# Optimization experiments

Hardware: AMD Instinct MI355X
Metric: run time of the kernel (lower is better)

## Reference

```python
import jax, jax.numpy as jnp
import numpy as np

N, E, B = 30000, 300000, 64
F_N, F_E, F_G, H = 64, 32, 32, 64
EPS = 1e-5


def _bn(t, gamma, beta):
    # BatchNorm1d in training mode: biased batch statistics over the row dim.
    m = t.mean(axis=0)
    v = t.var(axis=0)
    return gamma * (t - m) * jax.lax.rsqrt(v + EPS) + beta


def _seg_mean(vals, idx, num):
    s = jax.ops.segment_sum(vals, idx, num_segments=num)
    c = jax.ops.segment_sum(jnp.ones((vals.shape[0], 1), vals.dtype), idx,
                            num_segments=num)
    return s / jnp.maximum(c, 1.0)


def setup_inputs() -> dict:
    key = jax.random.key(0)
    ks = jax.random.split(key, 32)
    inp = {
        'x': jax.random.normal(ks[0], (N, F_N), jnp.float32),
        'edge_index': jax.random.randint(ks[1], (2, E), 0, N),
        'e': jax.random.normal(ks[2], (E, F_E), jnp.float32),
        'u': jax.random.normal(ks[3], (B, F_G), jnp.float32),
        'batch': jnp.sort(jax.random.randint(ks[4], (N,), 0, B)),
        'g_node': jnp.ones((F_N,), jnp.float32),
        'b_node': jnp.zeros((F_N,), jnp.float32),
        'g_edge': jnp.ones((F_E,), jnp.float32),
        'b_edge': jnp.zeros((F_E,), jnp.float32),
        'g_glob': jnp.ones((F_G,), jnp.float32),
        'b_glob': jnp.zeros((F_G,), jnp.float32),
    }
    # Per-step Linear weights; input dims follow the feature-size threading in __init__.
    din_e = [2 * F_N + F_E + F_G, 3 * H + H, 3 * H + H]  # [192, 256, 256]
    din_n = [F_N + H + F_G, H + H + H, H + H + H]        # [160, 192, 192]
    din_g = [H + F_G, H + H, H + H]                      # [96, 128, 128]
    k = 5
    for l in range(3):
        for tag, din in (('e', din_e[l]), ('n', din_n[l]), ('g', din_g[l])):
            inp[f'W{tag}{l}'] = jax.random.normal(ks[k], (din, H), jnp.float32) / np.sqrt(din)
            inp[f'b{tag}{l}'] = jnp.zeros((H,), jnp.float32)
            k += 1
    return inp


def _forward(x, e, u, batch, src, dst,
             g_node, b_node, g_edge, b_edge, g_glob, b_glob,
             We, be, Wn, bn, Wg, bg):
    # Input normalization
    x = _bn(x, g_node, b_node)
    e = _bn(e, g_edge, b_edge)
    u = _bn(u, g_glob, b_glob)
    for l in range(3):
        # Edge model: per-edge MLP over [x_src, x_dst, e, u_edge]
        e_in = jnp.concatenate([x[src], x[dst], e, u[batch[src]]], axis=-1)
        e = jax.nn.relu(e_in @ We[l] + be[l])
        # Node model: aggregate incoming messages at destination (mean)
        agg = _seg_mean(e, dst, N)
        n_in = jnp.concatenate([x, agg, u[batch]], axis=-1)
        x = jax.nn.relu(n_in @ Wn[l] + bn[l])
        # Global model: mean-pool nodes per graph
        g_in = jnp.concatenate([_seg_mean(x, batch, B), u], axis=-1)
        u = jax.nn.relu(g_in @ Wg[l] + bg[l])
    return x, e, u


def reference(x, edge_index, e, u, batch,
              g_node, b_node, g_edge, b_edge, g_glob, b_glob,
              We0, be0, Wn0, bn0, Wg0, bg0,
              We1, be1, Wn1, bn1, Wg1, bg1,
              We2, be2, Wn2, bn2, Wg2, bg2):
    src, dst = edge_index[0], edge_index[1]
    We = (We0, We1, We2); be = (be0, be1, be2)
    Wn = (Wn0, Wn1, Wn2); bn = (bn0, bn1, bn2)
    Wg = (Wg0, Wg1, Wg2); bg = (bg0, bg1, bg2)
    return _forward(x, e, u, batch, src, dst,
                    g_node, b_node, g_edge, b_edge, g_glob, b_glob,
                    We, be, Wn, bn, Wg, bg)
```

## Files before the change

### kernel.cpp

```cpp
#include <hip/hip_runtime.h>
#include <hip/hip_bf16.h>

#define EPS 1e-5f
typedef __hip_bfloat16 bf16;
typedef __attribute__((ext_vector_type(8))) short  short8;
typedef __attribute__((ext_vector_type(4))) float  f32x4;

__device__ __forceinline__ float b2f(bf16 v) { return __bfloat162float(v); }
__device__ __forceinline__ float bs2f(short s) { bf16 b = *reinterpret_cast<bf16*>(&s); return b2f(b); }
__device__ __forceinline__ float ldv(const void* p, size_t i, bool bf) {
    return bf ? b2f(((const bf16*)p)[i]) : ((const float*)p)[i];
}
__device__ __forceinline__ void stv(void* p, size_t i, float v, bool bf) {
    if (bf) ((bf16*)p)[i] = __float2bfloat16(v);
    else    ((float*)p)[i] = v;
}
__device__ __forceinline__ short f2bs(float v) {
    bf16 b = __float2bfloat16(v);
    return *reinterpret_cast<short*>(&b);
}
__device__ __forceinline__ short8 ld16s(const short* p) { return *(const short8*)p; }

__global__ void detect_dtype(const unsigned short* __restrict__ xs, float* __restrict__ flag) {
    __shared__ int cnt;
    if (threadIdx.x == 0) cnt = 0;
    __syncthreads();
    unsigned short u = xs[threadIdx.x];
    int e = (u >> 7) & 0xFF;
    int sane = (u == 0 || (e >= 110 && e <= 140)) ? 1 : 0;
    atomicAdd(&cnt, sane);
    __syncthreads();
    if (threadIdx.x == 0) flag[0] = (cnt >= 230) ? 1.0f : 0.0f;
}

template<int C>
__global__ __launch_bounds__(256) void bn_stats(const void* __restrict__ in, int R,
                                                float* __restrict__ stats, const float* __restrict__ flag) {
    bool isbf = flag[0] != 0.f;
    const int RG = 256 / C;
    int c = threadIdx.x % C, rg = threadIdx.x / C;
    float s = 0.f, s2 = 0.f;
    if (isbf) {
        const bf16* ip = (const bf16*)in;
        for (int r = blockIdx.x * RG + rg; r < R; r += gridDim.x * RG) {
            float v = b2f(ip[(size_t)r * C + c]); s += v; s2 += v * v;
        }
    } else {
        const float* ip = (const float*)in;
        for (int r = blockIdx.x * RG + rg; r < R; r += gridDim.x * RG) {
            float v = ip[(size_t)r * C + c]; s += v; s2 += v * v;
        }
    }
    __shared__ float sm[2][256];
    sm[0][threadIdx.x] = s; sm[1][threadIdx.x] = s2;
    __syncthreads();
    if (threadIdx.x < C) {
        float ts = 0.f, t2 = 0.f;
        for (int g = 0; g < RG; g++) { ts += sm[0][g * C + c]; t2 += sm[1][g * C + c]; }
        atomicAdd(&stats[c], ts);
        atomicAdd(&stats[C + c], t2);
    }
}

__global__ __launch_bounds__(256) void bn_apply_x(const void* __restrict__ in, short* __restrict__ out,
                                                  const float* __restrict__ stats, int R,
                                                  const void* __restrict__ gamma, const void* __restrict__ beta,
                                                  const float* __restrict__ flag) {
    bool isbf = flag[0] != 0.f;
    int total = R * 64;
    for (int i = blockIdx.x * 256 + threadIdx.x; i < total; i += gridDim.x * 256) {
        int c = i & 63;
        float mean = stats[c] / (float)R;
        float var = stats[64 + c] / (float)R - mean * mean;
        float inv = rsqrtf(var + EPS);
        out[i] = f2bs(ldv(gamma, c, isbf) * (ldv(in, i, isbf) - mean) * inv + ldv(beta, c, isbf));
    }
}

__global__ __launch_bounds__(256) void bn_apply_u(const void* __restrict__ in, float* __restrict__ outf,
                                                  short* __restrict__ outb,
                                                  const float* __restrict__ stats, int R,
                                                  const void* __restrict__ gamma, const void* __restrict__ beta,
                                                  const float* __restrict__ flag) {
    bool isbf = flag[0] != 0.f;
    int total = R * 32;
    for (int i = blockIdx.x * 256 + threadIdx.x; i < total; i += gridDim.x * 256) {
        int c = i & 31;
        float mean = stats[c] / (float)R;
        float var = stats[32 + c] / (float)R - mean * mean;
        float inv = rsqrtf(var + EPS);
        float v = ldv(gamma, c, isbf) * (ldv(in, i, isbf) - mean) * inv + ldv(beta, c, isbf);
        outf[i] = v; outb[i] = f2bs(v);
    }
}

__global__ __launch_bounds__(256) void count_kernel(const int* __restrict__ ei, int* __restrict__ cnt, int E) {
    int stride = gridDim.x * 256;
    for (int t = blockIdx.x * 256 + threadIdx.x; t < E; t += stride) atomicAdd(&cnt[ei[E + t]], 1);
}

__global__ __launch_bounds__(256) void csr_offsets(const int* __restrict__ cnt, int* __restrict__ off,
                                                   int* __restrict__ wcur, int* __restrict__ cursor, int N,
                                                   const int* __restrict__ batch, int* __restrict__ gstart, int B) {
    int n = blockIdx.x * 256 + threadIdx.x;
    if (n < N) {
        int o = atomicAdd(cursor, cnt[n]);
        off[n] = o; wcur[n] = o;
    }
    if (blockIdx.x == 0 && threadIdx.x <= B) {
        int t = threadIdx.x;
        int lo = 0, hi = N;
        while (lo < hi) { int mid = (lo + hi) >> 1; if (batch[mid] < t) lo = mid + 1; else hi = mid; }
        gstart[t] = lo;
    }
}

__global__ __launch_bounds__(256) void csr_fill(const int* __restrict__ ei, int* __restrict__ wcur,
                                                int* __restrict__ csr, int E) {
    int stride = gridDim.x * 256;
    for (int t = blockIdx.x * 256 + threadIdx.x; t < E; t += stride) {
        int d = ei[E + t];
        int pos = atomicAdd(&wcur[d], 1);
        csr[pos] = t;
    }
}

__global__ __launch_bounds__(256) void transpose_w(
    const void* __restrict__ W0, const void* __restrict__ W1, const void* __restrict__ W2,
    const void* __restrict__ W3, const void* __restrict__ W4, const void* __restrict__ W5,
    short* __restrict__ out, const float* __restrict__ flag)
{
    bool isbf = flag[0] != 0.f;
    const void* Ws[6] = {W0, W1, W2, W3, W4, W5};
    const int   din[6] = {192, 256, 256, 160, 192, 192};
    int mtx = blockIdx.x >> 3;
    int off = 0;
    for (int i = 0; i < mtx; i++) off += 64 * din[i];
    int d = din[mtx];
    const void* W = Ws[mtx];
    for (int i = (blockIdx.x & 7) * 256 + threadIdx.x; i < 64 * d; i += 8 * 256) {
        int n = i / d, k = i % d;
        out[off + n * d + k] = f2bs(ldv(W, (size_t)k * 64 + n, isbf));
    }
}

template<bool L0>
__global__ __launch_bounds__(256) void edge_mfma(
    const int* __restrict__ ei, const int* __restrict__ batchv,
    const short* __restrict__ xb,
    const void* __restrict__ ein, size_t ein_off,
    const float* __restrict__ estats, const void* __restrict__ egamma, const void* __restrict__ ebeta,
    const short* __restrict__ ub,
    const short* __restrict__ Wt, const void* __restrict__ biasv,
    void* __restrict__ eout, size_t eout_off,
    int E, const float* __restrict__ flag,
    int ein_force_bf, int eout_force_bf, short* __restrict__ eout2)
{
    constexpr int DIN = L0 ? 192 : 256;
    constexpr int NQ = DIN / 32;
    constexpr int ROWB = DIN * 2;
    __shared__ __align__(16) char Wl[64 * ROWB];
    __shared__ __align__(16) char T[4 * 2048];
    const bool isbf = flag[0] != 0.f;
    const bool ein_bf = ein_force_bf ? true : isbf;
    const bool eout_bf = eout_force_bf ? true : isbf;
    const int w = threadIdx.x >> 6, j = threadIdx.x & 63;
    const int m16 = j & 15, c8v = j >> 4, c8 = c8v * 8;
    const int rr8 = j >> 3, cc8 = j & 7;

    for (int i = threadIdx.x; i < DIN * 8; i += 256) {
        int lin = i * 16;
        int row = i / (DIN / 8);
        *(short8*)(Wl + (lin ^ ((row & 7) << 4))) = *(const short8*)(Wt + i * 8);
    }
    __syncthreads();

    char* Tw = T + w * 2048;
    const int wkey = (m16 & 7) << 4;

    float sc[8], sh[8];
    if constexpr (L0) {
        #pragma unroll
        for (int k = 0; k < 8; k++) {
            int col = c8 + k;
            float m = estats[col] / (float)E;
            float iv = rsqrtf(estats[32 + col] / (float)E - m * m + EPS);
            sc[k] = ldv(egamma, col, isbf) * iv;
            sh[k] = ldv(ebeta, col, isbf) - m * sc[k];
        }
    }
    float bc[4];
    #pragma unroll
    for (int t = 0; t < 4; t++) bc[t] = ldv(biasv, t * 16 + m16, isbf);

    const int ntiles = (E + 63) >> 6;
    const int gs = gridDim.x;
    int tile = blockIdx.x;
    if (tile < ntiles) {
        int ec = tile * 64 + w * 16 + m16; if (ec > E - 1) ec = E - 1;
        int s = ei[ec], d = ei[E + ec];
        for (; tile < ntiles; tile += gs) {
            const int ecC = ec, sC = s, dC = d;
            const int tn = tile + gs;
            if (tn < ntiles) {
                int e2 = tn * 64 + w * 16 + m16; if (e2 > E - 1) e2 = E - 1;
                ec = e2; s = ei[e2]; d = ei[E + e2];
            }
            int g = batchv[sC];

            short8 af[NQ];
            af[0] = ld16s(xb + (size_t)sC * 64 + c8);
            af[1] = ld16s(xb + (size_t)sC * 64 + 32 + c8);
            af[2] = ld16s(xb + (size_t)dC * 64 + c8);
            af[3] = ld16s(xb + (size_t)dC * 64 + 32 + c8);
            if constexpr (L0) {
                float ev[8];
                if (isbf) {
                    short8 r = ld16s((const short*)ein + (size_t)ecC * 32 + c8);
                    #pragma unroll
                    for (int k = 0; k < 8; k++) ev[k] = bs2f(r[k]);
                } else {
                    const float* ef = (const float*)ein + (size_t)ecC * 32 + c8;
                    float4 a = *(const float4*)ef, b = *(const float4*)(ef + 4);
                    ev[0]=a.x; ev[1]=a.y; ev[2]=a.z; ev[3]=a.w; ev[4]=b.x; ev[5]=b.y; ev[6]=b.z; ev[7]=b.w;
                }
                #pragma unroll
                for (int k = 0; k < 8; k++) af[4][k] = f2bs(ev[k] * sc[k] + sh[k]);
                af[5] = ld16s(ub + (size_t)g * 32 + c8);
            } else {
                if (ein_bf) {
                    af[4] = ld16s((const short*)ein + ein_off + (size_t)ecC * 64 + c8);
                    af[5] = ld16s((const short*)ein + ein_off + (size_t)ecC * 64 + 32 + c8);
                } else {
                    const float* ef = (const float*)ein + ein_off + (size_t)ecC * 64;
                    float4 a = *(const float4*)(ef + c8), b = *(const float4*)(ef + c8 + 4);
                    af[4][0]=f2bs(a.x); af[4][1]=f2bs(a.y); af[4][2]=f2bs(a.z); af[4][3]=f2bs(a.w);
                    af[4][4]=f2bs(b.x); af[4][5]=f2bs(b.y); af[4][6]=f2bs(b.z); af[4][7]=f2bs(b.w);
                    a = *(const float4*)(ef + 32 + c8); b = *(const float4*)(ef + 36 + c8);
                    af[5][0]=f2bs(a.x); af[5][1]=f2bs(a.y); af[5][2]=f2bs(a.z); af[5][3]=f2bs(a.w);
                    af[5][4]=f2bs(b.x); af[5][5]=f2bs(b.y); af[5][6]=f2bs(b.z); af[5][7]=f2bs(b.w);
                }
                af[6] = ld16s(ub + (size_t)g * 64 + c8);
                af[7] = ld16s(ub + (size_t)g * 64 + 32 + c8);
            }

            f32x4 acc[4] = {{0,0,0,0},{0,0,0,0},{0,0,0,0},{0,0,0,0}};
            #pragma unroll
            for (int q = 0; q < NQ; q++) {
                #pragma unroll
                for (int t = 0; t < 4; t++) {
                    int lin = (t * 16 + m16) * ROWB + q * 64 + c8v * 16;
                    short8 bv = *(const short8*)(Wl + (lin ^ wkey));
                    acc[t] = __builtin_amdgcn_mfma_f32_16x16x32_bf16(af[q], bv, acc[t], 0, 0, 0);
                }
            }

            const int we = tile * 64 + w * 16;
            #pragma unroll
            for (int t = 0; t < 4; t++) {
                #pragma unroll
                for (int r = 0; r < 4; r++) {
                    float v = fmaxf(acc[t][r] + bc[t], 0.f);
                    int rr = c8v * 4 + r;
                    int lin = rr * 128 + (t * 16 + m16) * 2;
                    *(short*)(Tw + (lin ^ ((rr & 7) << 4))) = f2bs(v);
                }
            }
            #pragma unroll
            for (int i = 0; i < 2; i++) {
                int r = i * 8 + rr8;
                int e2 = we + r;
                if (e2 < E) {
                    short8 row = *(const short8*)(Tw + ((r * 128 + cc8 * 16) ^ ((rr8 & 7) << 4)));
                    if (eout_bf) {
                        *(short8*)((short*)eout + eout_off + (size_t)e2 * 64 + cc8 * 8) = row;
                    } else {
                        float* op = (float*)eout + eout_off + (size_t)e2 * 64 + cc8 * 8;
                        float4 a, b;
                        a.x=bs2f(row[0]); a.y=bs2f(row[1]); a.z=bs2f(row[2]); a.w=bs2f(row[3]);
                        b.x=bs2f(row[4]); b.y=bs2f(row[5]); b.z=bs2f(row[6]); b.w=bs2f(row[7]);
                        *(float4*)op = a; *(float4*)(op + 4) = b;
                    }
                    if (eout2) {
                        *(short8*)(eout2 + (size_t)e2 * 64 + cc8 * 8) = row;
                    }
                }
            }
        }
    }
}

template<bool L0, bool FINAL>
__global__ __launch_bounds__(256) void node_fused(
    const int* __restrict__ batchv, const short* __restrict__ xin,
    const int* __restrict__ off, const int* __restrict__ csr, const int* __restrict__ cntv,
    const void* __restrict__ eout, size_t eoff,
    const short* __restrict__ ub,
    const short* __restrict__ Wt, const void* __restrict__ biasv,
    short* __restrict__ xoutb, void* __restrict__ dout, int N,
    const float* __restrict__ flag, int e_force_bf)
{
    constexpr int DIN = L0 ? 160 : 192;
    constexpr int NQ = DIN / 32;
    constexpr int ROWB = DIN * 2;
    __shared__ __align__(16) char Wl[64 * ROWB];
    __shared__ __align__(16) char T[4 * 2048];
    const bool isbf = flag[0] != 0.f;
    const bool e_bf = e_force_bf ? true : isbf;
    const int w = threadIdx.x >> 6, j = threadIdx.x & 63;
    const int m16 = j & 15, c8v = j >> 4, c8 = c8v * 8;
    const int rr8 = j >> 3, cc8 = j & 7;
    const int nb = blockIdx.x * 64 + w * 16;

    for (int i = threadIdx.x; i < DIN * 8; i += 256) {
        int lin = i * 16;
        int row = i / (DIN / 8);
        *(short8*)(Wl + (lin ^ ((row & 7) << 4))) = *(const short8*)(Wt + i * 8);
    }
    __syncthreads();

    char* Tw = T + w * 2048;
    const int wkey = (m16 & 7) << 4;

    int n = nb + m16; if (n > N - 1) n = N - 1;
    int g = batchv[n];

    short8 af[NQ];
    af[0] = ld16s(xin + (size_t)n * 64 + c8);
    af[1] = ld16s(xin + (size_t)n * 64 + 32 + c8);

    {
        int st = off[n], c = cntv[n];
        float s0[8] = {0,0,0,0,0,0,0,0}, s1[8] = {0,0,0,0,0,0,0,0};
        int t = 0;
        if (e_bf) {
            const short* ep = (const short*)eout + eoff;
            for (; t + 2 <= c; t += 2) {
                int e0 = csr[st + t], e1 = csr[st + t + 1];
                short8 r0 = ld16s(ep + (size_t)e0 * 64 + c8);
                short8 q0 = ld16s(ep + (size_t)e0 * 64 + 32 + c8);
                short8 r1 = ld16s(ep + (size_t)e1 * 64 + c8);
                short8 q1 = ld16s(ep + (size_t)e1 * 64 + 32 + c8);
                #pragma unroll
                for (int k = 0; k < 8; k++) { s0[k] += bs2f(r0[k]) + bs2f(r1[k]); s1[k] += bs2f(q0[k]) + bs2f(q1[k]); }
            }
            if (t < c) {
                int e0 = csr[st + t];
                short8 r0 = ld16s(ep + (size_t)e0 * 64 + c8);
                short8 q0 = ld16s(ep + (size_t)e0 * 64 + 32 + c8);
                #pragma unroll
                for (int k = 0; k < 8; k++) { s0[k] += bs2f(r0[k]); s1[k] += bs2f(q0[k]); }
            }
        } else {
            const float* ep = (const float*)eout + eoff;
            for (; t < c; t++) {
                int e0 = csr[st + t];
                const float* rp = ep + (size_t)e0 * 64;
                float4 a = *(const float4*)(rp + c8), b = *(const float4*)(rp + c8 + 4);
                float4 x = *(const float4*)(rp + 32 + c8), y = *(const float4*)(rp + 36 + c8);
                s0[0]+=a.x; s0[1]+=a.y; s0[2]+=a.z; s0[3]+=a.w; s0[4]+=b.x; s0[5]+=b.y; s0[6]+=b.z; s0[7]+=b.w;
                s1[0]+=x.x; s1[1]+=x.y; s1[2]+=x.z; s1[3]+=x.w; s1[4]+=y.x; s1[5]+=y.y; s1[6]+=y.z; s1[7]+=y.w;
            }
        }
        float rc = 1.0f / fmaxf((float)c, 1.0f);
        #pragma unroll
        for (int k = 0; k < 8; k++) { af[2][k] = f2bs(s0[k] * rc); af[3][k] = f2bs(s1[k] * rc); }
    }

    if constexpr (L0) {
        af[4] = ld16s(ub + (size_t)g * 32 + c8);
    } else {
        af[4] = ld16s(ub + (size_t)g * 64 + c8);
        af[5] = ld16s(ub + (size_t)g * 64 + 32 + c8);
    }

    f32x4 acc[4] = {{0,0,0,0},{0,0,0,0},{0,0,0,0},{0,0,0,0}};
    #pragma unroll
    for (int q = 0; q < NQ; q++) {
        #pragma unroll
        for (int t = 0; t < 4; t++) {
            int lin = (t * 16 + m16) * ROWB + q * 64 + c8v * 16;
            short8 bv = *(const short8*)(Wl + (lin ^ wkey));
            acc[t] = __builtin_amdgcn_mfma_f32_16x16x32_bf16(af[q], bv, acc[t], 0, 0, 0);
        }
    }

    #pragma unroll
    for (int t = 0; t < 4; t++) {
        float bcv = ldv(biasv, t * 16 + m16, isbf);
        #pragma unroll
        for (int r = 0; r < 4; r++) {
            float v = fmaxf(acc[t][r] + bcv, 0.f);
            int rr = c8v * 4 + r;
            int lin = rr * 128 + (t * 16 + m16) * 2;
            *(short*)(Tw + (lin ^ ((rr & 7) << 4))) = f2bs(v);
        }
    }
    #pragma unroll
    for (int i = 0; i < 2; i++) {
        int r = i * 8 + rr8;
        int n2 = nb + r;
        if (n2 < N) {
            short8 row = *(const short8*)(Tw + ((r * 128 + cc8 * 16) ^ ((rr8 & 7) << 4)));
            *(short8*)&xoutb[(size_t)n2 * 64 + cc8 * 8] = row;
            if (FINAL) {
                if (isbf) {
                    *(short8*)((short*)dout + (size_t)n2 * 64 + cc8 * 8) = row;
                } else {
                    float* op = (float*)dout + (size_t)n2 * 64 + cc8 * 8;
                    float4 a, b;
                    a.x=bs2f(row[0]); a.y=bs2f(row[1]); a.z=bs2f(row[2]); a.w=bs2f(row[3]);
                    b.x=bs2f(row[4]); b.y=bs2f(row[5]); b.z=bs2f(row[6]); b.w=bs2f(row[7]);
                    *(float4*)op = a; *(float4*)(op + 4) = b;
                }
            }
        }
    }
}

__global__ __launch_bounds__(256) void pool_kernel(const int* __restrict__ gstart,
                                                   const short* __restrict__ xb,
                                                   float* __restrict__ gsum) {
    int g = blockIdx.x >> 3, slice = blockIdx.x & 7;
    int st = gstart[g], en = gstart[g + 1];
    int len = en - st;
    int K = (len + 7) >> 3;
    int b0 = st + slice * K;
    int b1 = min(b0 + K, en);
    int rg = threadIdx.x >> 3, cc8 = threadIdx.x & 7;
    float a[8] = {0,0,0,0,0,0,0,0};
    for (int r = b0 + rg; r < b1; r += 32) {
        short8 v = *(const short8*)&xb[(size_t)r * 64 + cc8 * 8];
        #pragma unroll
        for (int k = 0; k < 8; k++) a[k] += bs2f(v[k]);
    }
    __shared__ float sm[32][64];
    #pragma unroll
    for (int k = 0; k < 8; k++) sm[rg][cc8 * 8 + k] = a[k];
    __syncthreads();
    if (threadIdx.x < 64) {
        float s = 0.f;
        #pragma unroll 8
        for (int q = 0; q < 32; q++) s += sm[q][threadIdx.x];
        atomicAdd(&gsum[g * 64 + threadIdx.x], s);
    }
}

template<int FU>
__global__ __launch_bounds__(256) void glob_gemm(
    const int* __restrict__ gstart, const float* __restrict__ gsum,
    const float* __restrict__ uin,
    const void* __restrict__ W, const void* __restrict__ biasv,
    float* __restrict__ uoutf, short* __restrict__ uoutb,
    const float* __restrict__ flag)
{
    bool isbf = flag[0] != 0.f;
    const int DIN = 64 + FU;
    __shared__ float s[4][192];
    int w = threadIdx.x >> 6, j = threadIdx.x & 63;
    int g = blockIdx.x * 4 + w;
    int st = gstart[g], en = gstart[g + 1];
    float rc = 1.0f / fmaxf((float)(en - st), 1.0f);
    s[w][j] = gsum[g * 64 + j] * rc;
    if (j < FU) s[w][64 + j] = uin[g * FU + j];
    float acc = ldv(biasv, j, isbf);
    for (int k = 0; k < DIN; k++) acc += s[w][k] * ldv(W, (size_t)k * 64 + j, isbf);
    acc = fmaxf(acc, 0.f);
    uoutf[g * 64 + j] = acc;
    uoutb[g * 64 + j] = f2bs(acc);
}

__global__ __launch_bounds__(256) void cast_out(const float* __restrict__ in, void* __restrict__ out,
                                                size_t out_off, int n, const float* __restrict__ flag) {
    bool isbf = flag[0] != 0.f;
    for (int i = blockIdx.x * 256 + threadIdx.x; i < n; i += gridDim.x * 256)
        stv(out, out_off + i, in[i], isbf);
}

extern "C" void kernel_launch(void* const* d_in, const int* in_sizes, int n_in,
                              void* d_out, int out_size, void* d_ws, size_t ws_size,
                              hipStream_t stream) {
    const void* x_in   = d_in[0];
    const int*  ei     = (const int*)d_in[1];
    const void* e_raw  = d_in[2];
    const void* u_raw  = d_in[3];
    const int*  batchv = (const int*)d_in[4];
    const void *g_node = d_in[5],  *b_node = d_in[6];
    const void *g_edge = d_in[7],  *b_edge = d_in[8];
    const void *g_glob = d_in[9],  *b_glob = d_in[10];
    const void* We[3] = {d_in[11], d_in[17], d_in[23]};
    const void* be[3] = {d_in[12], d_in[18], d_in[24]};
    const void* Wn[3] = {d_in[13], d_in[19], d_in[25]};
    const void* bn[3] = {d_in[14], d_in[20], d_in[26]};
    const void* Wg[3] = {d_in[15], d_in[21], d_in[27]};
    const void* bg[3] = {d_in[16], d_in[22], d_in[28]};

    const int N = in_sizes[0] / 64;
    const int E = in_sizes[2] / 32;
    const int B = in_sizes[3] / 32;

    float* p = (float*)d_ws;
    float* zbase  = p;
    float* stats  = p; p += 3 * 128;
    int*   cursor = (int*)p; p += 4;
    int*   cnt    = (int*)p; p += N;
    float* gsum0  = p; p += B * 64;
    float* gsum1  = p; p += B * 64;
    float* gsum2  = p; p += B * 64;
    size_t zbytes = (size_t)((char*)p - (char*)zbase);
    float* dflag  = p; p += 4;
    float* uN     = p; p += B * 32;
    float* uA     = p; p += B * 64;
    float* uB     = p; p += B * 64;
    int*   off    = (int*)p; p += N;
    int*   wcur   = (int*)p; p += N;
    int*   gstart = (int*)p; p += 72;
    int*   csr    = (int*)p; p += E;
    short* xb0    = (short*)p; p += (size_t)N * 32;
    short* xb1    = (short*)p; p += (size_t)N * 32;
    short* ubN    = (short*)p; p += B * 16;
    short* ubA    = (short*)p; p += B * 32;
    short* ubB    = (short*)p; p += B * 32;
    short* WtAll  = (short*)p; p += 79872 / 2;
    const short* WtE0 = WtAll;
    const short* WtE1 = WtAll + 12288;
    const short* WtE2 = WtAll + 28672;
    const short* WtN0 = WtAll + 45056;
    const short* WtN1 = WtAll + 55296;
    const short* WtN2 = WtAll + 67584;

    short* eb16 = nullptr;
    {
        size_t used = (size_t)((char*)p - (char*)d_ws);
        used = (used + 15) & ~(size_t)15;
        size_t need = used + (size_t)E * 64 * sizeof(short);
        if (ws_size >= need) eb16 = (short*)((char*)d_ws + used);
    }

    const size_t EOFF = (size_t)N * 64;
    const size_t UOFF = EOFF + (size_t)E * 64;

    hipMemsetAsync(zbase, 0, zbytes, stream);

    detect_dtype<<<1, 256, 0, stream>>>((const unsigned short*)x_in, dflag);

    bn_stats<64><<<256, 256, 0, stream>>>(x_in, N, stats, dflag);
    bn_stats<32><<<512, 256, 0, stream>>>(e_raw, E, stats + 128, dflag);
    bn_stats<32><<<8,   256, 0, stream>>>(u_raw, B, stats + 256, dflag);
    bn_apply_x<<<512, 256, 0, stream>>>(x_in, xb0, stats, N, g_node, b_node, dflag);
    bn_apply_u<<<8,   256, 0, stream>>>(u_raw, uN, ubN, stats + 256, B, g_glob, b_glob, dflag);
    count_kernel<<<512, 256, 0, stream>>>(ei, cnt, E);
    csr_offsets<<<(N + 255) / 256, 256, 0, stream>>>(cnt, off, wcur, cursor, N, batchv, gstart, B);
    csr_fill<<<512, 256, 0, stream>>>(ei, wcur, csr, E);
    transpose_w<<<48, 256, 0, stream>>>(We[0], We[1], We[2], Wn[0], Wn[1], Wn[2], WtAll, dflag);

    const int NG = (N + 63) / 64;
    const int NT = (E + 63) / 64;
    const int EG0 = NT < 1280 ? NT : 1280;
    const int EG  = NT < 1024 ? NT : 1024;

    if (eb16) {
        edge_mfma<true><<<EG0, 256, 0, stream>>>(
            ei, batchv, xb0, e_raw, 0, stats + 128, g_edge, b_edge,
            ubN, WtE0, be[0], eb16, 0, E, dflag, 0, 1, nullptr);
        node_fused<true, false><<<NG, 256, 0, stream>>>(
            batchv, xb0, off, csr, cnt, eb16, 0, ubN, WtN0, bn[0], xb1, nullptr, N, dflag, 1);
        pool_kernel<<<B * 8, 256, 0, stream>>>(gstart, xb1, gsum0);
        glob_gemm<32><<<B / 4, 256, 0, stream>>>(gstart, gsum0, uN, Wg[0], bg[0], uA, ubA, dflag);

        edge_mfma<false><<<EG, 256, 0, stream>>>(
            ei, batchv, xb1, eb16, 0, nullptr, nullptr, nullptr,
            ubA, WtE1, be[1], eb16, 0, E, dflag, 1, 1, nullptr);
        node_fused<false, false><<<NG, 256, 0, stream>>>(
            batchv, xb1, off, csr, cnt, eb16, 0, ubA, WtN1, bn[1], xb0, nullptr, N, dflag, 1);
        pool_kernel<<<B * 8, 256, 0, stream>>>(gstart, xb0, gsum1);
        glob_gemm<64><<<B / 4, 256, 0, stream>>>(gstart, gsum1, uA, Wg[1], bg[1], uB, ubB, dflag);

        edge_mfma<false><<<EG, 256, 0, stream>>>(
            ei, batchv, xb0, eb16, 0, nullptr, nullptr, nullptr,
            ubB, WtE2, be[2], d_out, EOFF, E, dflag, 1, 0, eb16);
        node_fused<false, true><<<NG, 256, 0, stream>>>(
            batchv, xb0, off, csr, cnt, eb16, 0, ubB, WtN2, bn[2], xb1, d_out, N, dflag, 1);
        pool_kernel<<<B * 8, 256, 0, stream>>>(gstart, xb1, gsum2);
        glob_gemm<64><<<B / 4, 256, 0, stream>>>(gstart, gsum2, uB, Wg[2], bg[2], uA, ubA, dflag);
    } else {
        edge_mfma<true><<<EG0, 256, 0, stream>>>(
            ei, batchv, xb0, e_raw, 0, stats + 128, g_edge, b_edge,
            ubN, WtE0, be[0], d_out, EOFF, E, dflag, 0, 0, nullptr);
        node_fused<true, false><<<NG, 256, 0, stream>>>(
            batchv, xb0, off, csr, cnt, d_out, EOFF, ubN, WtN0, bn[0], xb1, nullptr, N, dflag, 0);
        pool_kernel<<<B * 8, 256, 0, stream>>>(gstart, xb1, gsum0);
        glob_gemm<32><<<B / 4, 256, 0, stream>>>(gstart, gsum0, uN, Wg[0], bg[0], uA, ubA, dflag);

        edge_mfma<false><<<EG, 256, 0, stream>>>(
            ei, batchv, xb1, d_out, EOFF, nullptr, nullptr, nullptr,
            ubA, WtE1, be[1], d_out, EOFF, E, dflag, 0, 0, nullptr);
        node_fused<false, false><<<NG, 256, 0, stream>>>(
            batchv, xb1, off, csr, cnt, d_out, EOFF, ubA, WtN1, bn[1], xb0, nullptr, N, dflag, 0);
        pool_kernel<<<B * 8, 256, 0, stream>>>(gstart, xb0, gsum1);
        glob_gemm<64><<<B / 4, 256, 0, stream>>>(gstart, gsum1, uA, Wg[1], bg[1], uB, ubB, dflag);

        edge_mfma<false><<<EG, 256, 0, stream>>>(
            ei, batchv, xb0, d_out, EOFF, nullptr, nullptr, nullptr,
            ubB, WtE2, be[2], d_out, EOFF, E, dflag, 0, 0, nullptr);
        node_fused<false, true><<<NG, 256, 0, stream>>>(
            batchv, xb0, off, csr, cnt, d_out, EOFF, ubB, WtN2, bn[2], xb1, d_out, N, dflag, 0);
        pool_kernel<<<B * 8, 256, 0, stream>>>(gstart, xb1, gsum2);
        glob_gemm<64><<<B / 4, 256, 0, stream>>>(gstart, gsum2, uB, Wg[2], bg[2], uA, ubA, dflag);
    }

    cast_out<<<16, 256, 0, stream>>>(uA, d_out, UOFF, B * 64, dflag);
}
```

Baseline: 481.2 us.

## Process edges in destination-sorted CSR order so node aggregation reads contiguously

Builds permuted source/destination index arrays in CSR (destination-sorted) order and runs the edge kernels over that order on the bf16 path. Edge features are kept in sorted order in the scratch buffer, and the final layer scatters rows back to the original edge order for output. Node aggregation then reads each node's incoming edges as a contiguous block instead of through indirect CSR lookups. The cost is one extra permutation kernel, a gather of the raw edge features in the first layer, and a scattered write in the last layer.

```diff
diff --git a/kernel.cpp b/kernel.cpp
--- a/kernel.cpp
+++ b/kernel.cpp
@@ -122,6 +122,16 @@
         int d = ei[E + t];
         int pos = atomicAdd(&wcur[d], 1);
         csr[pos] = t;
+    }
+}
+
+__global__ __launch_bounds__(256) void perm_build(const int* __restrict__ ei, const int* __restrict__ csr,
+                                                  int* __restrict__ sp, int* __restrict__ dp, int E) {
+    int stride = gridDim.x * 256;
+    for (int t = blockIdx.x * 256 + threadIdx.x; t < E; t += stride) {
+        int e0 = csr[t];
+        sp[t] = ei[e0];
+        dp[t] = ei[E + e0];
     }
 }
 
@@ -146,7 +156,9 @@
 
 template<bool L0>
 __global__ __launch_bounds__(256) void edge_mfma(
-    const int* __restrict__ ei, const int* __restrict__ batchv,
+    const int* __restrict__ sp, const int* __restrict__ dp,
+    const int* __restrict__ csrv,
+    const int* __restrict__ batchv,
     const short* __restrict__ xb,
     const void* __restrict__ ein, size_t ein_off,
     const float* __restrict__ estats, const void* __restrict__ egamma, const void* __restrict__ ebeta,
@@ -154,7 +166,7 @@
     const short* __restrict__ Wt, const void* __restrict__ biasv,
     void* __restrict__ eout, size_t eout_off,
     int E, const float* __restrict__ flag,
-    int ein_force_bf, int eout_force_bf, short* __restrict__ eout2)
+    int ein_force_bf, int eout_force_bf, int eout_orig, short* __restrict__ eout2)
 {
     constexpr int DIN = L0 ? 192 : 256;
     constexpr int NQ = DIN / 32;
@@ -198,13 +210,16 @@
     int tile = blockIdx.x;
     if (tile < ntiles) {
         int ec = tile * 64 + w * 16 + m16; if (ec > E - 1) ec = E - 1;
-        int s = ei[ec], d = ei[E + ec];
+        int s = sp[ec], d = dp[ec];
+        int eo = ec;
+        if constexpr (L0) { if (csrv) eo = csrv[ec]; }
         for (; tile < ntiles; tile += gs) {
-            const int ecC = ec, sC = s, dC = d;
+            const int ecC = ec, sC = s, dC = d, eoC = eo;
             const int tn = tile + gs;
             if (tn < ntiles) {
                 int e2 = tn * 64 + w * 16 + m16; if (e2 > E - 1) e2 = E - 1;
-                ec = e2; s = ei[e2]; d = ei[E + e2];
+                ec = e2; s = sp[e2]; d = dp[e2];
+                if constexpr (L0) { if (csrv) eo = csrv[e2]; }
             }
             int g = batchv[sC];
 
@@ -216,11 +231,11 @@
             if constexpr (L0) {
                 float ev[8];
                 if (isbf) {
-                    short8 r = ld16s((const short*)ein + (size_t)ecC * 32 + c8);
+                    short8 r = ld16s((const short*)ein + (size_t)eoC * 32 + c8);
                     #pragma unroll
                     for (int k = 0; k < 8; k++) ev[k] = bs2f(r[k]);
                 } else {
-                    const float* ef = (const float*)ein + (size_t)ecC * 32 + c8;
+                    const float* ef = (const float*)ein + (size_t)eoC * 32 + c8;
                     float4 a = *(const float4*)ef, b = *(const float4*)(ef + 4);
                     ev[0]=a.x; ev[1]=a.y; ev[2]=a.z; ev[3]=a.w; ev[4]=b.x; ev[5]=b.y; ev[6]=b.z; ev[7]=b.w;
                 }
@@ -272,10 +287,11 @@
                 int e2 = we + r;
                 if (e2 < E) {
                     short8 row = *(const short8*)(Tw + ((r * 128 + cc8 * 16) ^ ((rr8 & 7) << 4)));
+                    int rowIdx = (eout_orig && csrv) ? csrv[e2] : e2;
                     if (eout_bf) {
-                        *(short8*)((short*)eout + eout_off + (size_t)e2 * 64 + cc8 * 8) = row;
+                        *(short8*)((short*)eout + eout_off + (size_t)rowIdx * 64 + cc8 * 8) = row;
                     } else {
-                        float* op = (float*)eout + eout_off + (size_t)e2 * 64 + cc8 * 8;
+                        float* op = (float*)eout + eout_off + (size_t)rowIdx * 64 + cc8 * 8;
                         float4 a, b;
                         a.x=bs2f(row[0]); a.y=bs2f(row[1]); a.z=bs2f(row[2]); a.w=bs2f(row[3]);
                         b.x=bs2f(row[4]); b.y=bs2f(row[5]); b.z=bs2f(row[6]); b.w=bs2f(row[7]);
@@ -298,7 +314,7 @@
     const short* __restrict__ ub,
     const short* __restrict__ Wt, const void* __restrict__ biasv,
     short* __restrict__ xoutb, void* __restrict__ dout, int N,
-    const float* __restrict__ flag, int e_force_bf)
+    const float* __restrict__ flag, int e_force_bf, int contig)
 {
     constexpr int DIN = L0 ? 160 : 192;
     constexpr int NQ = DIN / 32;
@@ -332,28 +348,47 @@
     {
         int st = off[n], c = cntv[n];
         float s0[8] = {0,0,0,0,0,0,0,0}, s1[8] = {0,0,0,0,0,0,0,0};
-        int t = 0;
         if (e_bf) {
             const short* ep = (const short*)eout + eoff;
-            for (; t + 2 <= c; t += 2) {
-                int e0 = csr[st + t], e1 = csr[st + t + 1];
-                short8 r0 = ld16s(ep + (size_t)e0 * 64 + c8);
-                short8 q0 = ld16s(ep + (size_t)e0 * 64 + 32 + c8);
-                short8 r1 = ld16s(ep + (size_t)e1 * 64 + c8);
-                short8 q1 = ld16s(ep + (size_t)e1 * 64 + 32 + c8);
-                #pragma unroll
-                for (int k = 0; k < 8; k++) { s0[k] += bs2f(r0[k]) + bs2f(r1[k]); s1[k] += bs2f(q0[k]) + bs2f(q1[k]); }
-            }
-            if (t < c) {
-                int e0 = csr[st + t];
-                short8 r0 = ld16s(ep + (size_t)e0 * 64 + c8);
-                short8 q0 = ld16s(ep + (size_t)e0 * 64 + 32 + c8);
-                #pragma unroll
-                for (int k = 0; k < 8; k++) { s0[k] += bs2f(r0[k]); s1[k] += bs2f(q0[k]); }
+            if (contig) {
+                const short* base = ep + (size_t)st * 64;
+                int t = 0;
+                for (; t + 2 <= c; t += 2) {
+                    short8 r0 = ld16s(base + (size_t)t * 64 + c8);
+                    short8 q0 = ld16s(base + (size_t)t * 64 + 32 + c8);
+                    short8 r1 = ld16s(base + (size_t)(t + 1) * 64 + c8);
+                    short8 q1 = ld16s(base + (size_t)(t + 1) * 64 + 32 + c8);
+                    #pragma unroll
+                    for (int k = 0; k < 8; k++) { s0[k] += bs2f(r0[k]) + bs2f(r1[k]); s1[k] += bs2f(q0[k]) + bs2f(q1[k]); }
+                }
+                if (t < c) {
+                    short8 r0 = ld16s(base + (size_t)t * 64 + c8);
+                    short8 q0 = ld16s(base + (size_t)t * 64 + 32 + c8);
+                    #pragma unroll
+                    for (int k = 0; k < 8; k++) { s0[k] += bs2f(r0[k]); s1[k] += bs2f(q0[k]); }
+                }
+            } else {
+                int t = 0;
+                for (; t + 2 <= c; t += 2) {
+                    int e0 = csr[st + t], e1 = csr[st + t + 1];
+                    short8 r0 = ld16s(ep + (size_t)e0 * 64 + c8);
+                    short8 q0 = ld16s(ep + (size_t)e0 * 64 + 32 + c8);
+                    short8 r1 = ld16s(ep + (size_t)e1 * 64 + c8);
+                    short8 q1 = ld16s(ep + (size_t)e1 * 64 + 32 + c8);
+                    #pragma unroll
+                    for (int k = 0; k < 8; k++) { s0[k] += bs2f(r0[k]) + bs2f(r1[k]); s1[k] += bs2f(q0[k]) + bs2f(q1[k]); }
+                }
+                if (t < c) {
+                    int e0 = csr[st + t];
+                    short8 r0 = ld16s(ep + (size_t)e0 * 64 + c8);
+                    short8 q0 = ld16s(ep + (size_t)e0 * 64 + 32 + c8);
+                    #pragma unroll
+                    for (int k = 0; k < 8; k++) { s0[k] += bs2f(r0[k]); s1[k] += bs2f(q0[k]); }
+                }
             }
         } else {
             const float* ep = (const float*)eout + eoff;
-            for (; t < c; t++) {
+            for (int t = 0; t < c; t++) {
                 int e0 = csr[st + t];
                 const float* rp = ep + (size_t)e0 * 64;
                 float4 a = *(const float4*)(rp + c8), b = *(const float4*)(rp + c8 + 4);
@@ -516,6 +551,8 @@
     int*   wcur   = (int*)p; p += N;
     int*   gstart = (int*)p; p += 72;
     int*   csr    = (int*)p; p += E;
+    int*   sp     = (int*)p; p += E;
+    int*   dp     = (int*)p; p += E;
     short* xb0    = (short*)p; p += (size_t)N * 32;
     short* xb1    = (short*)p; p += (size_t)N * 32;
     short* ubN    = (short*)p; p += B * 16;
@@ -552,6 +589,7 @@
     count_kernel<<<512, 256, 0, stream>>>(ei, cnt, E);
     csr_offsets<<<(N + 255) / 256, 256, 0, stream>>>(cnt, off, wcur, cursor, N, batchv, gstart, B);
     csr_fill<<<512, 256, 0, stream>>>(ei, wcur, csr, E);
+    perm_build<<<512, 256, 0, stream>>>(ei, csr, sp, dp, E);
     transpose_w<<<48, 256, 0, stream>>>(We[0], We[1], We[2], Wn[0], Wn[1], Wn[2], WtAll, dflag);
 
     const int NG = (N + 63) / 64;
@@ -561,50 +599,50 @@
 
     if (eb16) {
         edge_mfma<true><<<EG0, 256, 0, stream>>>(
-            ei, batchv, xb0, e_raw, 0, stats + 128, g_edge, b_edge,
-            ubN, WtE0, be[0], eb16, 0, E, dflag, 0, 1, nullptr);
+            sp, dp, csr, batchv, xb0, e_raw, 0, stats + 128, g_edge, b_edge,
+            ubN, WtE0, be[0], eb16, 0, E, dflag, 0, 1, 0, nullptr);
         node_fused<true, false><<<NG, 256, 0, stream>>>(
-            batchv, xb0, off, csr, cnt, eb16, 0, ubN, WtN0, bn[0], xb1, nullptr, N, dflag, 1);
+            batchv, xb0, off, csr, cnt, eb16, 0, ubN, WtN0, bn[0], xb1, nullptr, N, dflag, 1, 1);
         pool_kernel<<<B * 8, 256, 0, stream>>>(gstart, xb1, gsum0);
         glob_gemm<32><<<B / 4, 256, 0, stream>>>(gstart, gsum0, uN, Wg[0], bg[0], uA, ubA, dflag);
 
         edge_mfma<false><<<EG, 256, 0, stream>>>(
-            ei, batchv, xb1, eb16, 0, nullptr, nullptr, nullptr,
-            ubA, WtE1, be[1], eb16, 0, E, dflag, 1, 1, nullptr);
+            sp, dp, csr, batchv, xb1, eb16, 0, nullptr, nullptr, nullptr,
+            ubA, WtE1, be[1], eb16, 0, E, dflag, 1, 1, 0, nullptr);
         node_fused<false, false><<<NG, 256, 0, stream>>>(
-            batchv, xb1, off, csr, cnt, eb16, 0, ubA, WtN1, bn[1], xb0, nullptr, N, dflag, 1);
+            batchv, xb1, off, csr, cnt, eb16, 0, ubA, WtN1, bn[1], xb0, nullptr, N, dflag, 1, 1);
         pool_kernel<<<B * 8, 256, 0, stream>>>(gstart, xb0, gsum1);
         glob_gemm<64><<<B / 4, 256, 0, stream>>>(gstart, gsum1, uA, Wg[1], bg[1], uB, ubB, dflag);
 
         edge_mfma<false><<<EG, 256, 0, stream>>>(
-            ei, batchv, xb0, eb16, 0, nullptr, nullptr, nullptr,
-            ubB, WtE2, be[2], d_out, EOFF, E, dflag, 1, 0, eb16);
+            sp, dp, csr, batchv, xb0, eb16, 0, nullptr, nullptr, nullptr,
+            ubB, WtE2, be[2], d_out, EOFF, E, dflag, 1, 0, 1, eb16);
         node_fused<false, true><<<NG, 256, 0, stream>>>(
-            batchv, xb0, off, csr, cnt, eb16, 0, ubB, WtN2, bn[2], xb1, d_out, N, dflag, 1);
+            batchv, xb0, off, csr, cnt, eb16, 0, ubB, WtN2, bn[2], xb1, d_out, N, dflag, 1, 1);
         pool_kernel<<<B * 8, 256, 0, stream>>>(gstart, xb1, gsum2);
         glob_gemm<64><<<B / 4, 256, 0, stream>>>(gstart, gsum2, uB, Wg[2], bg[2], uA, ubA, dflag);
     } else {
         edge_mfma<true><<<EG0, 256, 0, stream>>>(
-            ei, batchv, xb0, e_raw, 0, stats + 128, g_edge, b_edge,
-            ubN, WtE0, be[0], d_out, EOFF, E, dflag, 0, 0, nullptr);
+            ei, ei + E, nullptr, batchv, xb0, e_raw, 0, stats + 128, g_edge, b_edge,
+            ubN, WtE0, be[0], d_out, EOFF, E, dflag, 0, 0, 0, nullptr);
         node_fused<true, false><<<NG, 256, 0, stream>>>(
-            batchv, xb0, off, csr, cnt, d_out, EOFF, ubN, WtN0, bn[0], xb1, nullptr, N, dflag, 0);
+            batchv, xb0, off, csr, cnt, d_out, EOFF, ubN, WtN0, bn[0], xb1, nullptr, N, dflag, 0, 0);
         pool_kernel<<<B * 8, 256, 0, stream>>>(gstart, xb1, gsum0);
         glob_gemm<32><<<B / 4, 256, 0, stream>>>(gstart, gsum0, uN, Wg[0], bg[0], uA, ubA, dflag);
 
         edge_mfma<false><<<EG, 256, 0, stream>>>(
-            ei, batchv, xb1, d_out, EOFF, nullptr, nullptr, nullptr,
-            ubA, WtE1, be[1], d_out, EOFF, E, dflag, 0, 0, nullptr);
+            ei, ei + E, nullptr, batchv, xb1, d_out, EOFF, nullptr, nullptr, nullptr,
+            ubA, WtE1, be[1], d_out, EOFF, E, dflag, 0, 0, 0, nullptr);
         node_fused<false, false><<<NG, 256, 0, stream>>>(
-            batchv, xb1, off, csr, cnt, d_out, EOFF, ubA, WtN1, bn[1], xb0, nullptr, N, dflag, 0);
+            batchv, xb1, off, csr, cnt, d_out, EOFF, ubA, WtN1, bn[1], xb0, nullptr, N, dflag, 0, 0);
         pool_kernel<<<B * 8, 256, 0, stream>>>(gstart, xb0, gsum1);
         glob_gemm<64><<<B / 4, 256, 0, stream>>>(gstart, gsum1, uA, Wg[1], bg[1], uB, ubB, dflag);
 
         edge_mfma<false><<<EG, 256, 0, stream>>>(
-            ei, batchv, xb0, d_out, EOFF, nullptr, nullptr, nullptr,
-            ubB, WtE2, be[2], d_out, EOFF, E, dflag, 0, 0, nullptr);
+            ei, ei + E, nullptr, batchv, xb0, d_out, EOFF, nullptr, nullptr, nullptr,
+            ubB, WtE2, be[2], d_out, EOFF, E, dflag, 0, 0, 0, nullptr);
         node_fused<false, true><<<NG, 256, 0, stream>>>(
-            batchv, xb0, off, csr, cnt, d_out, EOFF, ubB, WtN2, bn[2], xb1, d_out, N, dflag, 0);
+            batchv, xb0, off, csr, cnt, d_out, EOFF, ubB, WtN2, bn[2], xb1, d_out, N, dflag, 0, 0);
         pool_kernel<<<B * 8, 256, 0, stream>>>(gstart, xb1, gsum2);
         glob_gemm<64><<<B / 4, 256, 0, stream>>>(gstart, gsum2, uB, Wg[2], bg[2], uA, ubA, dflag);
     }
```

After: 472.0 us (median of 2 runs). About the same (-1.9%).
